# Performance work log

Hardware: AMD Instinct MI355X
Metric: run time of the kernel (lower is better)

The kernel has to match this reference:

```python
import jax, jax.numpy as jnp
import numpy as np

N_DIM = 512
HEADS = 8
NUM_EXPERTS = 65536
NUM_KEYS = 256      # sqrt(NUM_EXPERTS)
DIM_KEY = 256       # N_DIM // 2
TOPK = 16           # num_experts_per_head (also product_key_topk)
SCALE = 0.02


def setup_inputs() -> dict:
    key = jax.random.key(0)
    k0, k1, k2, k3, k4 = jax.random.split(key, 5)
    x = jax.random.normal(k0, (1, 2048, N_DIM), dtype=jnp.float32)
    W_q = jax.random.normal(k1, (N_DIM, 2 * HEADS * DIM_KEY), dtype=jnp.float32) * SCALE
    keys = jax.random.normal(k2, (HEADS, NUM_KEYS, 2, DIM_KEY), dtype=jnp.float32) * SCALE
    down_embed = jax.random.normal(k3, (NUM_EXPERTS, N_DIM), dtype=jnp.float32) * SCALE
    up_embed = jax.random.normal(k4, (NUM_EXPERTS, N_DIM), dtype=jnp.float32) * SCALE
    return {"x": x, "W_q": W_q, "keys": keys, "down_embed": down_embed, "up_embed": up_embed}


def reference(x, W_q, keys, down_embed, up_embed):
    b, n, d = x.shape
    # queries: [b,n,2*h*dk] -> [2,b,n,h,dk]
    q = (x @ W_q).reshape(b, n, 2, HEADS, DIM_KEY).transpose(2, 0, 1, 3, 4)
    # similarity against product keys: [2,b,n,h,num_keys]
    sim = jnp.einsum('pbnhd,hkpd->pbnhk', q, keys)
    sx, ix = jax.lax.top_k(sim[0], TOPK)   # [b,n,h,TOPK]
    sy, iy = jax.lax.top_k(sim[1], TOPK)
    # cartesian product of the two top-k sets -> [b,n,h,TOPK*TOPK]
    all_scores = (sx[..., :, None] + sy[..., None, :]).reshape(b, n, HEADS, TOPK * TOPK)
    scores, pk_idx = jax.lax.top_k(all_scores, TOPK)  # [b,n,h,TOPK]
    # NOTE: original module indexes embeddings with pk_idx (flat top-k positions),
    # reproduced faithfully here.
    w_down = down_embed[pk_idx]  # [b,n,h,TOPK,d]
    w_up = up_embed[pk_idx]      # [b,n,h,TOPK,d]
    h = jnp.einsum('bnd,bnhkd->bnhk', x, w_down)
    h = jax.nn.gelu(h, approximate=False)
    h = jax.nn.softmax(scores, axis=-1) * h
    return jnp.einsum('bnhk,bnhkd->bnd', h, w_up)
```

## Files before the change

kernel.cpp:

```cpp
#include <hip/hip_runtime.h>
#include <math.h>

#define N_TOK 2048
#define NDIM 512
#define HEADS 8
#define TOPK 16
#define QCOLS 4096
#define LSC 4096.0f
#define ILSC (1.0f/4096.0f)

typedef __attribute__((ext_vector_type(8))) _Float16 f16x8;
typedef __attribute__((ext_vector_type(4))) float f32x4;

__device__ __forceinline__ unsigned short f32_to_f16(float f) {
    _Float16 h = (_Float16)f;
    return __builtin_bit_cast(unsigned short, h);
}
__device__ __forceinline__ float f16_to_f32(unsigned short u) {
    return (float)__builtin_bit_cast(_Float16, u);
}
__device__ __forceinline__ void gl_lds16(const void* g, void* l) {
    __builtin_amdgcn_global_load_lds(
        (const __attribute__((address_space(1))) void*)g,
        (__attribute__((address_space(3))) void*)l, 16, 0, 0);
}

__device__ __forceinline__ void split_f4(const float* __restrict__ src,
                                         unsigned short* __restrict__ dh,
                                         unsigned short* __restrict__ dl,
                                         int i) {
    float4 v = reinterpret_cast<const float4*>(src)[i];
    float vv[4] = {v.x, v.y, v.z, v.w};
    ushort4 h, lo;
    unsigned short* hp = &h.x; unsigned short* lp = &lo.x;
    #pragma unroll
    for (int q = 0; q < 4; ++q) {
        unsigned short hh = f32_to_f16(vv[q]);
        hp[q] = hh;
        lp[q] = f32_to_f16((vv[q] - f16_to_f32(hh)) * LSC);
    }
    reinterpret_cast<ushort4*>(dh)[i] = h;
    reinterpret_cast<ushort4*>(dl)[i] = lo;
}

__global__ __launch_bounds__(256) void kP_split(const float* __restrict__ x,
                                                const float* __restrict__ Wq,
                                                const float* __restrict__ keys,
                                                const float* __restrict__ down,
                                                const float* __restrict__ up,
                                                unsigned short* __restrict__ xh,
                                                unsigned short* __restrict__ xl,
                                                unsigned short* __restrict__ Wqh,
                                                unsigned short* __restrict__ Wql,
                                                unsigned short* __restrict__ ksh,
                                                unsigned short* __restrict__ ksl,
                                                unsigned short* __restrict__ Mth,
                                                unsigned short* __restrict__ Mtl,
                                                unsigned short* __restrict__ upTh,
                                                unsigned short* __restrict__ upTl) {
    const int bid = blockIdx.x;
    const int tid = threadIdx.x;
    if (bid < 256) {
        #pragma unroll
        for (int t = 0; t < 4; ++t) split_f4(x, xh, xl, bid * 1024 + t * 256 + tid);
        return;
    }
    if (bid < 768) {
        const int b = bid - 256;
        #pragma unroll
        for (int t = 0; t < 4; ++t) split_f4(Wq, Wqh, Wql, b * 1024 + t * 256 + tid);
        return;
    }
    if (bid < 1024) {
        const int b = bid - 768;
        #pragma unroll
        for (int t = 0; t < 4; ++t) split_f4(keys, ksh, ksl, b * 1024 + t * 256 + tid);
        return;
    }
    if (bid < 1280) {
        const int e = bid - 1024;
        const int d0 = tid * 2;
        float2 v = *reinterpret_cast<const float2*>(&down[(size_t)e * NDIM + d0]);
        ushort2 h, lo;
        unsigned short h0 = f32_to_f16(v.x);
        unsigned short h1 = f32_to_f16(v.y);
        h.x = h0; h.y = h1;
        lo.x = f32_to_f16((v.x - f16_to_f32(h0)) * LSC);
        lo.y = f32_to_f16((v.y - f16_to_f32(h1)) * LSC);
        *reinterpret_cast<ushort2*>(&Mth[(size_t)(QCOLS + e) * NDIM + d0]) = h;
        *reinterpret_cast<ushort2*>(&Mtl[(size_t)(QCOLS + e) * NDIM + d0]) = lo;
        return;
    }
    const int b = bid - 1280;
    #pragma unroll
    for (int dd = 0; dd < 8; ++dd) {
        const int d = b * 8 + dd;
        const int e = tid;
        const float v = up[(size_t)e * NDIM + d];
        unsigned short hh = f32_to_f16(v);
        upTh[(size_t)d * 256 + e] = hh;
        upTl[(size_t)d * 256 + e] = f32_to_f16((v - f16_to_f32(hh)) * LSC);
    }
}

__global__ __launch_bounds__(256) void kQ_m1(const unsigned short* __restrict__ Wqh,
                                             const unsigned short* __restrict__ Wql,
                                             const unsigned short* __restrict__ ksh,
                                             const unsigned short* __restrict__ ksl,
                                             unsigned short* __restrict__ Mth,
                                             unsigned short* __restrict__ Mtl) {
    __shared__ __align__(16) char lds[36864];
    const int tid = threadIdx.x;
    const int w = tid >> 6, l = tid & 63;
    const int c0 = blockIdx.x * 32;
    const int ph = blockIdx.y;
    const int p = ph >> 3, h = ph & 7;
    const int off = p * 2048 + h * 256;
    f32x4 acch[2][4] = {};
    f32x4 accl[2][4] = {};

    for (int s = 0; s < 8; ++s) {
        const int kk = s * 32;
        __syncthreads();
        {
            const int q = w * 1024 + l * 16;
            const int r = q >> 7;
            const int bsw = (q & 127) ^ ((r & 7) << 4);
            const unsigned short* src = (bsw < 64)
                ? Wqh + (size_t)(c0 + r) * QCOLS + off + kk + (bsw >> 1)
                : Wql + (size_t)(c0 + r) * QCOLS + off + kk + ((bsw - 64) >> 1);
            gl_lds16(src, lds + w * 1024);
        }
        #pragma unroll
        for (int t = 0; t < 8; ++t) {
            const int q = w * 8192 + t * 1024 + l * 16;
            const int r = q >> 7;
            const int bsw = (q & 127) ^ ((r & 7) << 4);
            const unsigned short* src = (bsw < 64)
                ? ksh + ((size_t)(h * 256 + r) * 2 + p) * 256 + kk + (bsw >> 1)
                : ksl + ((size_t)(h * 256 + r) * 2 + p) * 256 + kk + ((bsw - 64) >> 1);
            gl_lds16(src, lds + 4096 + w * 8192 + t * 1024);
        }
        __syncthreads();
        const int bq = (l >> 4) * 16;
        f16x8 ah[2], al[2];
        #pragma unroll
        for (int mi = 0; mi < 2; ++mi) {
            const int ra = mi * 16 + (l & 15);
            const int swz = (ra & 7) << 4;
            ah[mi] = *(const f16x8*)(lds + ra * 128 + (bq ^ swz));
            al[mi] = *(const f16x8*)(lds + ra * 128 + ((bq + 64) ^ swz));
        }
        __builtin_amdgcn_s_setprio(1);
        #pragma unroll
        for (int nj = 0; nj < 4; ++nj) {
            const int rb = w * 64 + nj * 16 + (l & 15);
            const int swz = (rb & 7) << 4;
            f16x8 bh = *(const f16x8*)(lds + 4096 + rb * 128 + (bq ^ swz));
            f16x8 bl = *(const f16x8*)(lds + 4096 + rb * 128 + ((bq + 64) ^ swz));
            #pragma unroll
            for (int mi = 0; mi < 2; ++mi) {
                acch[mi][nj] = __builtin_amdgcn_mfma_f32_16x16x32_f16(ah[mi], bh, acch[mi][nj], 0, 0, 0);
                accl[mi][nj] = __builtin_amdgcn_mfma_f32_16x16x32_f16(ah[mi], bl, accl[mi][nj], 0, 0, 0);
                accl[mi][nj] = __builtin_amdgcn_mfma_f32_16x16x32_f16(al[mi], bh, accl[mi][nj], 0, 0, 0);
            }
        }
        __builtin_amdgcn_s_setprio(0);
    }
    #pragma unroll
    for (int mi = 0; mi < 2; ++mi)
        #pragma unroll
        for (int nj = 0; nj < 4; ++nj) {
            const int k = w * 64 + nj * 16 + (l & 15);
            const int cb = c0 + mi * 16 + (l >> 4) * 4;
            ushort4 h4, l4;
            unsigned short* hp = &h4.x; unsigned short* lp = &l4.x;
            #pragma unroll
            for (int r = 0; r < 4; ++r) {
                const float v = fmaf(accl[mi][nj][r], ILSC, acch[mi][nj][r]);
                unsigned short hh = f32_to_f16(v);
                hp[r] = hh;
                lp[r] = f32_to_f16((v - f16_to_f32(hh)) * LSC);
            }
            *reinterpret_cast<ushort4*>(&Mth[(size_t)(off + k) * NDIM + cb]) = h4;
            *reinterpret_cast<ushort4*>(&Mtl[(size_t)(off + k) * NDIM + cb]) = l4;
        }
}

#define BM 128
#define BN 128
#define BK 32
#define KFBUF 32768
__global__ __launch_bounds__(256, 2) void kF_gemm(const unsigned short* __restrict__ xh,
                                                  const unsigned short* __restrict__ xl,
                                                  const unsigned short* __restrict__ Mth,
                                                  const unsigned short* __restrict__ Mtl,
                                                  float* __restrict__ T,
                                                  float* __restrict__ D) {
    __shared__ __align__(16) char lds[2 * KFBUF];
    const int tid = threadIdx.x;
    const int w = tid >> 6, l = tid & 63;
    const int wm = w >> 1, wn = w & 1;
    const int orig = blockIdx.x;
    const int swz = (orig & 7) * 68 + (orig >> 3);
    const int by = swz >> 4;
    const int row0 = (swz & 15) * BM;
    const int colbase = by * 128;
    f32x4 acch[4][4] = {};
    f32x4 accl[4][4] = {};

    auto stage = [&](int buf, int s) {
        const int kk = s * BK;
        char* base = lds + buf * KFBUF;
        #pragma unroll
        for (int t = 0; t < 4; ++t) {
            const int q = w * 4096 + t * 1024 + l * 16;
            const int r = q >> 7;
            const int bsw = (q & 127) ^ ((r & 7) << 4);
            const unsigned short* src = (bsw < 64)
                ? xh + (size_t)(row0 + r) * NDIM + kk + (bsw >> 1)
                : xl + (size_t)(row0 + r) * NDIM + kk + ((bsw - 64) >> 1);
            gl_lds16(src, base + w * 4096 + t * 1024);
        }
        #pragma unroll
        for (int t = 0; t < 4; ++t) {
            const int q = w * 4096 + t * 1024 + l * 16;
            const int r = q >> 7;
            const int bsw = (q & 127) ^ ((r & 7) << 4);
            const unsigned short* src = (bsw < 64)
                ? Mth + (size_t)(colbase + r) * NDIM + kk + (bsw >> 1)
                : Mtl + (size_t)(colbase + r) * NDIM + kk + ((bsw - 64) >> 1);
            gl_lds16(src, base + 16384 + w * 4096 + t * 1024);
        }
    };

    stage(0, 0);
    __syncthreads();
    for (int s = 0; s < 16; ++s) {
        if (s + 1 < 16) stage((s + 1) & 1, s + 1);
        const char* base = lds + (s & 1) * KFBUF;
        const int bq = (l >> 4) * 16;
        f16x8 bh[4], bl[4];
        #pragma unroll
        for (int nj = 0; nj < 4; ++nj) {
            const int rb = wn * 64 + nj * 16 + (l & 15);
            const int sz = (rb & 7) << 4;
            bh[nj] = *(const f16x8*)(base + 16384 + rb * 128 + (bq ^ sz));
            bl[nj] = *(const f16x8*)(base + 16384 + rb * 128 + ((bq + 64) ^ sz));
        }
        __builtin_amdgcn_s_setprio(1);
        #pragma unroll
        for (int mi = 0; mi < 4; ++mi) {
            const int ra = wm * 64 + mi * 16 + (l & 15);
            const int sz = (ra & 7) << 4;
            f16x8 ah = *(const f16x8*)(base + ra * 128 + (bq ^ sz));
            f16x8 al = *(const f16x8*)(base + ra * 128 + ((bq + 64) ^ sz));
            #pragma unroll
            for (int nj = 0; nj < 4; ++nj) {
                acch[mi][nj] = __builtin_amdgcn_mfma_f32_16x16x32_f16(ah, bh[nj], acch[mi][nj], 0, 0, 0);
                accl[mi][nj] = __builtin_amdgcn_mfma_f32_16x16x32_f16(ah, bl[nj], accl[mi][nj], 0, 0, 0);
                accl[mi][nj] = __builtin_amdgcn_mfma_f32_16x16x32_f16(al, bh[nj], accl[mi][nj], 0, 0, 0);
            }
        }
        __builtin_amdgcn_s_setprio(0);
        __syncthreads();
    }

    if (by >= 32) {
        #pragma unroll
        for (int mi = 0; mi < 4; ++mi)
            #pragma unroll
            for (int nj = 0; nj < 4; ++nj)
                #pragma unroll
                for (int r = 0; r < 4; ++r) {
                    const int row = row0 + wm * 64 + mi * 16 + (l >> 4) * 4 + r;
                    const int col = (by - 32) * 128 + wn * 64 + nj * 16 + (l & 15);
                    D[(size_t)row * 256 + col] = fmaf(accl[mi][nj][r], ILSC, acch[mi][nj][r]);
                }
        return;
    }

    float* Cl = (float*)lds;
    const int grp8 = tid >> 3;
    const int lam8 = tid & 7;
    for (int c = 0; c < 4; ++c) {
        if (wm == (c >> 1)) {
            #pragma unroll
            for (int u = 0; u < 2; ++u) {
                const int mi = (c & 1) * 2 + u;
                #pragma unroll
                for (int nj = 0; nj < 4; ++nj)
                    #pragma unroll
                    for (int r = 0; r < 4; ++r)
                        Cl[(u * 16 + (l >> 4) * 4 + r) * 136 + wn * 64 + nj * 16 + (l & 15)] =
                            fmaf(accl[mi][nj][r], ILSC, acch[mi][nj][r]);
            }
        }
        __syncthreads();
        float v[16];
        #pragma unroll
        for (int j = 0; j < 16; ++j) v[j] = Cl[grp8 * 136 + lam8 + 8 * j];
        #pragma unroll
        for (int k = 2; k <= 16; k <<= 1)
            #pragma unroll
            for (int j = k >> 1; j > 0; j >>= 1)
                #pragma unroll
                for (int i = 0; i < 16; ++i) {
                    const int l2 = i ^ j;
                    if (l2 > i) {
                        const bool asc = ((i & k) == 0);
                        const float lo = fminf(v[i], v[l2]), hi = fmaxf(v[i], v[l2]);
                        v[i] = asc ? lo : hi;
                        v[l2] = asc ? hi : lo;
                    }
                }
        #pragma unroll
        for (int lvl = 1; lvl <= 4; lvl <<= 1) {
            float m[16];
            #pragma unroll
            for (int q = 0; q < 16; ++q)
                m[q] = fmaxf(v[q], __shfl_xor(v[15 - q], lvl));
            #pragma unroll
            for (int j = 8; j > 0; j >>= 1)
                #pragma unroll
                for (int i = 0; i < 16; ++i) {
                    const int l2 = i ^ j;
                    if (l2 > i) {
                        const float lo = fminf(m[i], m[l2]), hi = fmaxf(m[i], m[l2]);
                        m[i] = lo; m[l2] = hi;
                    }
                }
            #pragma unroll
            for (int q = 0; q < 16; ++q) v[q] = m[q];
        }
        const int n = row0 + c * 32 + grp8;
        T[((size_t)n * 32 + by) * 16 + 2 * lam8]     = v[15 - 2 * lam8];
        T[((size_t)n * 32 + by) * 16 + 2 * lam8 + 1] = v[14 - 2 * lam8];
        __syncthreads();
    }
}

__device__ const unsigned short CAND_TBL[32] = {
    0x0100, 0x0302, 0x0504, 0x0706, 0x0908, 0x0B0A, 0x0D0C, 0x0F0E,
    0x1110, 0x1312, 0x1514, 0x1716,
    0x2120, 0x2322, 0x3024, 0x3231, 0x4033, 0x4241,
    0x5150, 0x6160, 0x7170,
    0x9080, 0xB0A0, 0xD0C0, 0xF0E0,
    0xFFFF, 0xFFFF, 0xFFFF, 0xFFFF, 0xFFFF, 0xFFFF, 0xFFFF
};

__device__ __forceinline__ float sel16(const float a[16], int i) {
    float b0 = (i & 1) ? a[1] : a[0];
    float b1 = (i & 1) ? a[3] : a[2];
    float b2 = (i & 1) ? a[5] : a[4];
    float b3 = (i & 1) ? a[7] : a[6];
    float b4 = (i & 1) ? a[9] : a[8];
    float b5 = (i & 1) ? a[11] : a[10];
    float b6 = (i & 1) ? a[13] : a[12];
    float b7 = (i & 1) ? a[15] : a[14];
    float c0 = (i & 2) ? b1 : b0;
    float c1 = (i & 2) ? b3 : b2;
    float c2 = (i & 2) ? b5 : b4;
    float c3 = (i & 2) ? b7 : b6;
    float d0 = (i & 4) ? c1 : c0;
    float d1 = (i & 4) ? c3 : c2;
    return (i & 8) ? d1 : d0;
}

__device__ __forceinline__ void merge_desc16(const float* __restrict__ a,
                                             const float* __restrict__ b,
                                             float out_desc[16]) {
    float m[16];
    #pragma unroll
    for (int q = 0; q < 16; ++q) m[q] = fmaxf(a[q], b[15 - q]);
    #pragma unroll
    for (int k = 2; k <= 16; k <<= 1)
        #pragma unroll
        for (int j = k >> 1; j > 0; j >>= 1)
            #pragma unroll
            for (int i = 0; i < 16; ++i) {
                const int l2 = i ^ j;
                if (l2 > i) {
                    const bool asc = ((i & k) == 0);
                    const float lo = fminf(m[i], m[l2]), hi = fmaxf(m[i], m[l2]);
                    m[i] = asc ? lo : hi;
                    m[l2] = asc ? hi : lo;
                }
            }
    #pragma unroll
    for (int q = 0; q < 16; ++q) out_desc[q] = m[15 - q];
}

__global__ __launch_bounds__(256) void kC_combine(const float* __restrict__ T,
                                                  const float* __restrict__ D,
                                                  unsigned short* __restrict__ Wh,
                                                  unsigned short* __restrict__ Wl) {
    __shared__ unsigned long long ckey[8][50];
    __shared__ float winval[8][16];
    __shared__ int winflat[8][16];
    __shared__ int Wrow[256];

    const int tid = threadIdx.x;
    const int n = blockIdx.x;
    const int h = tid >> 5;
    const int lam = tid & 15;

    Wrow[tid] = 0;

    float a0[16], a1[16], b0v[16], b1v[16];
    const float* t00 = &T[((size_t)n * 32 + 2 * h) * 16];
    const float* t01 = &T[((size_t)n * 32 + 2 * h + 1) * 16];
    const float* t10 = &T[((size_t)n * 32 + 16 + 2 * h) * 16];
    const float* t11 = &T[((size_t)n * 32 + 17 + 2 * h) * 16];
    #pragma unroll
    for (int q = 0; q < 16; ++q) {
        a0[q] = t00[q]; a1[q] = t01[q];
        b0v[q] = t10[q]; b1v[q] = t11[q];
    }
    float sxd[16], syd[16];
    merge_desc16(a0, a1, sxd);
    merge_desc16(b0v, b1v, syd);

    const int lc = tid & 31;
    const unsigned int cw = CAND_TBL[lc];
    unsigned long long mykey[2]; float myval[2]; int myflat[2]; int myrank[2] = {0, 0};
    #pragma unroll
    for (int u = 0; u < 2; ++u) {
        const int fl = (cw >> (8 * u)) & 0xFF;
        const float sv = sel16(sxd, fl >> 4) + sel16(syd, fl & 15);
        const unsigned int uv = __float_as_uint(sv);
        const unsigned int mo = (uv & 0x80000000u) ? ~uv : (uv | 0x80000000u);
        mykey[u] = ((unsigned long long)mo << 8) | (unsigned long long)(255 - fl);
        myval[u] = sv; myflat[u] = fl;
        const int slot = lc * 2 + u;
        if (slot < 50) ckey[h][slot] = mykey[u];
    }
    __syncthreads();
    for (int kk = 0; kk < 50; ++kk) {
        const unsigned long long ok = ckey[h][kk];
        myrank[0] += (ok > mykey[0]) ? 1 : 0;
        myrank[1] += (ok > mykey[1]) ? 1 : 0;
    }
    #pragma unroll
    for (int u = 0; u < 2; ++u)
        if (myrank[u] < 16) { winval[h][myrank[u]] = myval[u]; winflat[h][myrank[u]] = myflat[u]; }
    __syncthreads();

    if (!(tid & 16)) {
        const float sc = winval[h][lam];
        const float m0 = winval[h][0];
        float e = expf(sc - m0);
        float esum = e;
        #pragma unroll
        for (int off = 1; off < 16; off <<= 1) esum += __shfl_xor(esum, off);
        const int fl = winflat[h][lam];
        const float hv = D[(size_t)n * 256 + fl];
        const float gg = 0.5f * hv * (1.0f + erff(hv * 0.70710678118654752f));
        const float wv = (e / esum) * gg;
        atomicAdd(&Wrow[fl], __float2int_rn(wv * 4194304.0f));
    }
    __syncthreads();
    const float wfin = (float)Wrow[tid] * (1.0f / 4194304.0f);
    const unsigned short hh = f32_to_f16(wfin);
    Wh[(size_t)n * 256 + tid] = hh;
    Wl[(size_t)n * 256 + tid] = f32_to_f16((wfin - f16_to_f32(hh)) * LSC);
}

__global__ __launch_bounds__(256) void k5_mfma(const unsigned short* __restrict__ Wh,
                                               const unsigned short* __restrict__ Wl,
                                               const unsigned short* __restrict__ upTh,
                                               const unsigned short* __restrict__ upTl,
                                               float* __restrict__ out) {
    __shared__ __align__(16) char lds[20480];
    const int tid = threadIdx.x;
    const int w = tid >> 6, l = tid & 63;
    const int n0 = blockIdx.x * 32;
    const int d0 = blockIdx.y * 128;
    f32x4 acch[2][2] = {};
    f32x4 accl[2][2] = {};

    for (int s = 0; s < 8; ++s) {
        const int kk = s * 32;
        __syncthreads();
        {
            const int q = w * 1024 + l * 16;
            const int r = q >> 7;
            const int bsw = (q & 127) ^ ((r & 7) << 4);
            const unsigned short* src = (bsw < 64)
                ? Wh + (size_t)(n0 + r) * 256 + kk + (bsw >> 1)
                : Wl + (size_t)(n0 + r) * 256 + kk + ((bsw - 64) >> 1);
            gl_lds16(src, lds + w * 1024);
        }
        #pragma unroll
        for (int t = 0; t < 4; ++t) {
            const int q = w * 4096 + t * 1024 + l * 16;
            const int r = q >> 7;
            const int bsw = (q & 127) ^ ((r & 7) << 4);
            const unsigned short* src = (bsw < 64)
                ? upTh + (size_t)(d0 + r) * 256 + kk + (bsw >> 1)
                : upTl + (size_t)(d0 + r) * 256 + kk + ((bsw - 64) >> 1);
            gl_lds16(src, lds + 4096 + w * 4096 + t * 1024);
        }
        __syncthreads();
        const int bq = (l >> 4) * 16;
        f16x8 ah[2], al[2];
        #pragma unroll
        for (int mi = 0; mi < 2; ++mi) {
            const int ra = mi * 16 + (l & 15);
            const int swz = (ra & 7) << 4;
            ah[mi] = *(const f16x8*)(lds + ra * 128 + (bq ^ swz));
            al[mi] = *(const f16x8*)(lds + ra * 128 + ((bq + 64) ^ swz));
        }
        #pragma unroll
        for (int nj = 0; nj < 2; ++nj) {
            const int rb = w * 32 + nj * 16 + (l & 15);
            const int swz = (rb & 7) << 4;
            f16x8 bh = *(const f16x8*)(lds + 4096 + rb * 128 + (bq ^ swz));
            f16x8 bl = *(const f16x8*)(lds + 4096 + rb * 128 + ((bq + 64) ^ swz));
            #pragma unroll
            for (int mi = 0; mi < 2; ++mi) {
                acch[mi][nj] = __builtin_amdgcn_mfma_f32_16x16x32_f16(ah[mi], bh, acch[mi][nj], 0, 0, 0);
                accl[mi][nj] = __builtin_amdgcn_mfma_f32_16x16x32_f16(ah[mi], bl, accl[mi][nj], 0, 0, 0);
                accl[mi][nj] = __builtin_amdgcn_mfma_f32_16x16x32_f16(al[mi], bh, accl[mi][nj], 0, 0, 0);
            }
        }
    }
    #pragma unroll
    for (int mi = 0; mi < 2; ++mi)
        #pragma unroll
        for (int nj = 0; nj < 2; ++nj)
            #pragma unroll
            for (int r = 0; r < 4; ++r) {
                const int row = n0 + mi * 16 + (l >> 4) * 4 + r;
                const int col = d0 + w * 32 + nj * 16 + (l & 15);
                out[(size_t)row * NDIM + col] = fmaf(accl[mi][nj][r], ILSC, acch[mi][nj][r]);
            }
}

extern "C" void kernel_launch(void* const* d_in, const int* in_sizes, int n_in,
                              void* d_out, int out_size, void* d_ws, size_t ws_size,
                              hipStream_t stream) {
    const float* x    = (const float*)d_in[0];
    const float* Wq   = (const float*)d_in[1];
    const float* keys = (const float*)d_in[2];
    const float* down = (const float*)d_in[3];
    const float* up   = (const float*)d_in[4];
    float* out = (float*)d_out;

    char* ws = (char*)d_ws;
    unsigned short* Mth  = (unsigned short*)(ws);
    unsigned short* Mtl  = (unsigned short*)(ws + 4456448);
    unsigned short* xh   = (unsigned short*)(ws + 8912896);
    unsigned short* xl   = (unsigned short*)(ws + 11010048);
    unsigned short* Wqh  = (unsigned short*)(ws + 13107200);
    unsigned short* Wql  = (unsigned short*)(ws + 17301504);
    unsigned short* ksh  = (unsigned short*)(ws + 21495808);
    unsigned short* ksl  = (unsigned short*)(ws + 23592960);
    unsigned short* upTh = (unsigned short*)(ws + 25690112);
    unsigned short* upTl = (unsigned short*)(ws + 25952256);
    float* T             = (float*)(ws + 26214400);
    float* D             = (float*)(ws + 30408704);
    unsigned short* Wh   = (unsigned short*)(ws + 32505856);
    unsigned short* Wl   = (unsigned short*)(ws + 33554432);

    kP_split<<<1344, 256, 0, stream>>>(x, Wq, keys, down, up,
                                       xh, xl, Wqh, Wql, ksh, ksl, Mth, Mtl, upTh, upTl);
    kQ_m1<<<dim3(16, 16), 256, 0, stream>>>(Wqh, Wql, ksh, ksl, Mth, Mtl);
    kF_gemm<<<544, 256, 0, stream>>>(xh, xl, Mth, Mtl, T, D);
    kC_combine<<<2048, 256, 0, stream>>>(T, D, Wh, Wl);
    k5_mfma<<<dim3(64, 4), 256, 0, stream>>>(Wh, Wl, upTh, upTl, out);
}
```

Baseline: 100.3 us.

## Pre-swizzle split-f16 operands into LDS tile layout and merge accumulators

Result: faster. 94.49 us (-5.8%).

```diff
diff --git a/kernel.cpp b/kernel.cpp
--- a/kernel.cpp
+++ b/kernel.cpp
@@ -25,10 +25,10 @@
         (__attribute__((address_space(3))) void*)l, 16, 0, 0);
 }
 
-__device__ __forceinline__ void split_f4(const float* __restrict__ src,
-                                         unsigned short* __restrict__ dh,
-                                         unsigned short* __restrict__ dl,
-                                         int i) {
+__device__ __forceinline__ void split_f4s(const float* __restrict__ src,
+                                          unsigned short* __restrict__ dh,
+                                          unsigned short* __restrict__ dl,
+                                          int i, float lsc) {
     float4 v = reinterpret_cast<const float4*>(src)[i];
     float vv[4] = {v.x, v.y, v.z, v.w};
     ushort4 h, lo;
@@ -37,7 +37,7 @@
     for (int q = 0; q < 4; ++q) {
         unsigned short hh = f32_to_f16(vv[q]);
         hp[q] = hh;
-        lp[q] = f32_to_f16((vv[q] - f16_to_f32(hh)) * LSC);
+        lp[q] = f32_to_f16((vv[q] - f16_to_f32(hh)) * lsc);
     }
     reinterpret_cast<ushort4*>(dh)[i] = h;
     reinterpret_cast<ushort4*>(dl)[i] = lo;
@@ -48,33 +48,51 @@
                                                 const float* __restrict__ keys,
                                                 const float* __restrict__ down,
                                                 const float* __restrict__ up,
-                                                unsigned short* __restrict__ xh,
-                                                unsigned short* __restrict__ xl,
+                                                char* __restrict__ xc,
                                                 unsigned short* __restrict__ Wqh,
                                                 unsigned short* __restrict__ Wql,
                                                 unsigned short* __restrict__ ksh,
                                                 unsigned short* __restrict__ ksl,
-                                                unsigned short* __restrict__ Mth,
-                                                unsigned short* __restrict__ Mtl,
+                                                char* __restrict__ Mc,
                                                 unsigned short* __restrict__ upTh,
                                                 unsigned short* __restrict__ upTl) {
     const int bid = blockIdx.x;
     const int tid = threadIdx.x;
     if (bid < 256) {
         #pragma unroll
-        for (int t = 0; t < 4; ++t) split_f4(x, xh, xl, bid * 1024 + t * 256 + tid);
+        for (int t = 0; t < 4; ++t) {
+            const int i = bid * 1024 + t * 256 + tid;
+            float4 v = reinterpret_cast<const float4*>(x)[i];
+            float vv[4] = {v.x, v.y, v.z, v.w};
+            ushort4 h, lo;
+            unsigned short* hp = &h.x; unsigned short* lp = &lo.x;
+            #pragma unroll
+            for (int q = 0; q < 4; ++q) {
+                unsigned short hh = f32_to_f16(vv[q]);
+                hp[q] = hh;
+                lp[q] = f32_to_f16(vv[q] - f16_to_f32(hh));
+            }
+            const int n = i >> 7;
+            const int k0 = (i & 127) * 4;
+            const int s = k0 >> 5;
+            const int o = (k0 & 31) * 2;
+            const int swz = (n & 7) << 4;
+            char* base = xc + ((size_t)s * 2048 + n) * 128;
+            *reinterpret_cast<ushort4*>(base + (o ^ swz)) = h;
+            *reinterpret_cast<ushort4*>(base + ((64 + o) ^ swz)) = lo;
+        }
         return;
     }
     if (bid < 768) {
         const int b = bid - 256;
         #pragma unroll
-        for (int t = 0; t < 4; ++t) split_f4(Wq, Wqh, Wql, b * 1024 + t * 256 + tid);
+        for (int t = 0; t < 4; ++t) split_f4s(Wq, Wqh, Wql, b * 1024 + t * 256 + tid, LSC);
         return;
     }
     if (bid < 1024) {
         const int b = bid - 768;
         #pragma unroll
-        for (int t = 0; t < 4; ++t) split_f4(keys, ksh, ksl, b * 1024 + t * 256 + tid);
+        for (int t = 0; t < 4; ++t) split_f4s(keys, ksh, ksl, b * 1024 + t * 256 + tid, LSC);
         return;
     }
     if (bid < 1280) {
@@ -85,10 +103,15 @@
         unsigned short h0 = f32_to_f16(v.x);
         unsigned short h1 = f32_to_f16(v.y);
         h.x = h0; h.y = h1;
-        lo.x = f32_to_f16((v.x - f16_to_f32(h0)) * LSC);
-        lo.y = f32_to_f16((v.y - f16_to_f32(h1)) * LSC);
-        *reinterpret_cast<ushort2*>(&Mth[(size_t)(QCOLS + e) * NDIM + d0]) = h;
-        *reinterpret_cast<ushort2*>(&Mtl[(size_t)(QCOLS + e) * NDIM + d0]) = lo;
+        lo.x = f32_to_f16(v.x - f16_to_f32(h0));
+        lo.y = f32_to_f16(v.y - f16_to_f32(h1));
+        const int s = d0 >> 5;
+        const int o = (d0 & 31) * 2;
+        const int mrow = QCOLS + e;
+        const int swz = (mrow & 7) << 4;
+        char* base = Mc + ((size_t)s * 4352 + mrow) * 128;
+        *reinterpret_cast<ushort2*>(base + (o ^ swz)) = h;
+        *reinterpret_cast<ushort2*>(base + ((64 + o) ^ swz)) = lo;
         return;
     }
     const int b = bid - 1280;
@@ -107,8 +130,7 @@
                                              const unsigned short* __restrict__ Wql,
                                              const unsigned short* __restrict__ ksh,
                                              const unsigned short* __restrict__ ksl,
-                                             unsigned short* __restrict__ Mth,
-                                             unsigned short* __restrict__ Mtl) {
+                                             char* __restrict__ Mc) {
     __shared__ __align__(16) char lds[36864];
     const int tid = threadIdx.x;
     const int w = tid >> 6, l = tid & 63;
@@ -180,10 +202,15 @@
                 const float v = fmaf(accl[mi][nj][r], ILSC, acch[mi][nj][r]);
                 unsigned short hh = f32_to_f16(v);
                 hp[r] = hh;
-                lp[r] = f32_to_f16((v - f16_to_f32(hh)) * LSC);
-            }
-            *reinterpret_cast<ushort4*>(&Mth[(size_t)(off + k) * NDIM + cb]) = h4;
-            *reinterpret_cast<ushort4*>(&Mtl[(size_t)(off + k) * NDIM + cb]) = l4;
+                lp[r] = f32_to_f16(v - f16_to_f32(hh));
+            }
+            const int mrow = off + k;
+            const int s2 = cb >> 5;
+            const int o = (cb & 31) * 2;
+            const int swz2 = (mrow & 7) << 4;
+            char* base = Mc + ((size_t)s2 * 4352 + mrow) * 128;
+            *reinterpret_cast<ushort4*>(base + (o ^ swz2)) = h4;
+            *reinterpret_cast<ushort4*>(base + ((64 + o) ^ swz2)) = l4;
         }
 }
 
@@ -191,10 +218,8 @@
 #define BN 128
 #define BK 32
 #define KFBUF 32768
-__global__ __launch_bounds__(256, 2) void kF_gemm(const unsigned short* __restrict__ xh,
-                                                  const unsigned short* __restrict__ xl,
-                                                  const unsigned short* __restrict__ Mth,
-                                                  const unsigned short* __restrict__ Mtl,
+__global__ __launch_bounds__(256, 2) void kF_gemm(const char* __restrict__ xc,
+                                                  const char* __restrict__ Mc,
                                                   float* __restrict__ T,
                                                   float* __restrict__ D) {
     __shared__ __align__(16) char lds[2 * KFBUF];
@@ -206,31 +231,16 @@
     const int by = swz >> 4;
     const int row0 = (swz & 15) * BM;
     const int colbase = by * 128;
-    f32x4 acch[4][4] = {};
-    f32x4 accl[4][4] = {};
+    f32x4 acc[4][4] = {};
 
     auto stage = [&](int buf, int s) {
-        const int kk = s * BK;
         char* base = lds + buf * KFBUF;
+        const char* asrc = xc + ((size_t)s * 2048 + row0) * 128;
+        const char* bsrc = Mc + ((size_t)s * 4352 + colbase) * 128;
         #pragma unroll
         for (int t = 0; t < 4; ++t) {
-            const int q = w * 4096 + t * 1024 + l * 16;
-            const int r = q >> 7;
-            const int bsw = (q & 127) ^ ((r & 7) << 4);
-            const unsigned short* src = (bsw < 64)
-                ? xh + (size_t)(row0 + r) * NDIM + kk + (bsw >> 1)
-                : xl + (size_t)(row0 + r) * NDIM + kk + ((bsw - 64) >> 1);
-            gl_lds16(src, base + w * 4096 + t * 1024);
-        }
-        #pragma unroll
-        for (int t = 0; t < 4; ++t) {
-            const int q = w * 4096 + t * 1024 + l * 16;
-            const int r = q >> 7;
-            const int bsw = (q & 127) ^ ((r & 7) << 4);
-            const unsigned short* src = (bsw < 64)
-                ? Mth + (size_t)(colbase + r) * NDIM + kk + (bsw >> 1)
-                : Mtl + (size_t)(colbase + r) * NDIM + kk + ((bsw - 64) >> 1);
-            gl_lds16(src, base + 16384 + w * 4096 + t * 1024);
+            gl_lds16(asrc + t * 4096 + tid * 16, base + t * 4096 + tid * 16);
+            gl_lds16(bsrc + t * 4096 + tid * 16, base + 16384 + t * 4096 + tid * 16);
         }
     };
 
@@ -257,9 +267,9 @@
             f16x8 al = *(const f16x8*)(base + ra * 128 + ((bq + 64) ^ sz));
             #pragma unroll
             for (int nj = 0; nj < 4; ++nj) {
-                acch[mi][nj] = __builtin_amdgcn_mfma_f32_16x16x32_f16(ah, bh[nj], acch[mi][nj], 0, 0, 0);
-                accl[mi][nj] = __builtin_amdgcn_mfma_f32_16x16x32_f16(ah, bl[nj], accl[mi][nj], 0, 0, 0);
-                accl[mi][nj] = __builtin_amdgcn_mfma_f32_16x16x32_f16(al, bh[nj], accl[mi][nj], 0, 0, 0);
+                acc[mi][nj] = __builtin_amdgcn_mfma_f32_16x16x32_f16(ah, bh[nj], acc[mi][nj], 0, 0, 0);
+                acc[mi][nj] = __builtin_amdgcn_mfma_f32_16x16x32_f16(ah, bl[nj], acc[mi][nj], 0, 0, 0);
+                acc[mi][nj] = __builtin_amdgcn_mfma_f32_16x16x32_f16(al, bh[nj], acc[mi][nj], 0, 0, 0);
             }
         }
         __builtin_amdgcn_s_setprio(0);
@@ -275,7 +285,7 @@
                 for (int r = 0; r < 4; ++r) {
                     const int row = row0 + wm * 64 + mi * 16 + (l >> 4) * 4 + r;
                     const int col = (by - 32) * 128 + wn * 64 + nj * 16 + (l & 15);
-                    D[(size_t)row * 256 + col] = fmaf(accl[mi][nj][r], ILSC, acch[mi][nj][r]);
+                    D[(size_t)row * 256 + col] = acc[mi][nj][r];
                 }
         return;
     }
@@ -283,6 +293,7 @@
     float* Cl = (float*)lds;
     const int grp8 = tid >> 3;
     const int lam8 = tid & 7;
+    #pragma unroll
     for (int c = 0; c < 4; ++c) {
         if (wm == (c >> 1)) {
             #pragma unroll
@@ -293,49 +304,51 @@
                     #pragma unroll
                     for (int r = 0; r < 4; ++r)
                         Cl[(u * 16 + (l >> 4) * 4 + r) * 136 + wn * 64 + nj * 16 + (l & 15)] =
-                            fmaf(accl[mi][nj][r], ILSC, acch[mi][nj][r]);
-            }
-        }
-        __syncthreads();
-        float v[16];
-        #pragma unroll
-        for (int j = 0; j < 16; ++j) v[j] = Cl[grp8 * 136 + lam8 + 8 * j];
-        #pragma unroll
-        for (int k = 2; k <= 16; k <<= 1)
-            #pragma unroll
-            for (int j = k >> 1; j > 0; j >>= 1)
+                            acc[mi][nj][r];
+            }
+        }
+        __syncthreads();
+        {
+            float v[16];
+            #pragma unroll
+            for (int j = 0; j < 16; ++j) v[j] = Cl[grp8 * 136 + lam8 + 8 * j];
+            #pragma unroll
+            for (int k = 2; k <= 16; k <<= 1)
                 #pragma unroll
-                for (int i = 0; i < 16; ++i) {
-                    const int l2 = i ^ j;
-                    if (l2 > i) {
-                        const bool asc = ((i & k) == 0);
-                        const float lo = fminf(v[i], v[l2]), hi = fmaxf(v[i], v[l2]);
-                        v[i] = asc ? lo : hi;
-                        v[l2] = asc ? hi : lo;
+                for (int j = k >> 1; j > 0; j >>= 1)
+                    #pragma unroll
+                    for (int i = 0; i < 16; ++i) {
+                        const int l2 = i ^ j;
+                        if (l2 > i) {
+                            const bool asc = ((i & k) == 0);
+                            const float lo = fminf(v[i], v[l2]), hi = fmaxf(v[i], v[l2]);
+                            v[i] = asc ? lo : hi;
+                            v[l2] = asc ? hi : lo;
+                        }
                     }
-                }
-        #pragma unroll
-        for (int lvl = 1; lvl <= 4; lvl <<= 1) {
-            float m[16];
-            #pragma unroll
-            for (int q = 0; q < 16; ++q)
-                m[q] = fmaxf(v[q], __shfl_xor(v[15 - q], lvl));
-            #pragma unroll
-            for (int j = 8; j > 0; j >>= 1)
+            #pragma unroll
+            for (int lvl = 1; lvl <= 4; lvl <<= 1) {
+                float m[16];
                 #pragma unroll
-                for (int i = 0; i < 16; ++i) {
-                    const int l2 = i ^ j;
-                    if (l2 > i) {
-                        const float lo = fminf(m[i], m[l2]), hi = fmaxf(m[i], m[l2]);
-                        m[i] = lo; m[l2] = hi;
+                for (int q = 0; q < 16; ++q)
+                    m[q] = fmaxf(v[q], __shfl_xor(v[15 - q], lvl));
+                #pragma unroll
+                for (int j = 8; j > 0; j >>= 1)
+                    #pragma unroll
+                    for (int i = 0; i < 16; ++i) {
+                        const int l2 = i ^ j;
+                        if (l2 > i) {
+                            const float lo = fminf(m[i], m[l2]), hi = fmaxf(m[i], m[l2]);
+                            m[i] = lo; m[l2] = hi;
+                        }
                     }
-                }
-            #pragma unroll
-            for (int q = 0; q < 16; ++q) v[q] = m[q];
-        }
-        const int n = row0 + c * 32 + grp8;
-        T[((size_t)n * 32 + by) * 16 + 2 * lam8]     = v[15 - 2 * lam8];
-        T[((size_t)n * 32 + by) * 16 + 2 * lam8 + 1] = v[14 - 2 * lam8];
+                #pragma unroll
+                for (int q = 0; q < 16; ++q) v[q] = m[q];
+            }
+            const int n = row0 + c * 32 + grp8;
+            T[((size_t)n * 32 + by) * 16 + 2 * lam8]     = v[15 - 2 * lam8];
+            T[((size_t)n * 32 + by) * 16 + 2 * lam8 + 1] = v[14 - 2 * lam8];
+        }
         __syncthreads();
     }
 }
@@ -548,10 +561,8 @@
     float* out = (float*)d_out;
 
     char* ws = (char*)d_ws;
-    unsigned short* Mth  = (unsigned short*)(ws);
-    unsigned short* Mtl  = (unsigned short*)(ws + 4456448);
-    unsigned short* xh   = (unsigned short*)(ws + 8912896);
-    unsigned short* xl   = (unsigned short*)(ws + 11010048);
+    char* Mc             = ws;
+    char* xc             = ws + 8912896;
     unsigned short* Wqh  = (unsigned short*)(ws + 13107200);
     unsigned short* Wql  = (unsigned short*)(ws + 17301504);
     unsigned short* ksh  = (unsigned short*)(ws + 21495808);
@@ -564,9 +575,9 @@
     unsigned short* Wl   = (unsigned short*)(ws + 33554432);
 
     kP_split<<<1344, 256, 0, stream>>>(x, Wq, keys, down, up,
-                                       xh, xl, Wqh, Wql, ksh, ksl, Mth, Mtl, upTh, upTl);
-    kQ_m1<<<dim3(16, 16), 256, 0, stream>>>(Wqh, Wql, ksh, ksl, Mth, Mtl);
-    kF_gemm<<<544, 256, 0, stream>>>(xh, xl, Mth, Mtl, T, D);
+                                       xc, Wqh, Wql, ksh, ksl, Mc, upTh, upTl);
+    kQ_m1<<<dim3(16, 16), 256, 0, stream>>>(Wqh, Wql, ksh, ksl, Mc);
+    kF_gemm<<<544, 256, 0, stream>>>(xc, Mc, T, D);
     kC_combine<<<2048, 256, 0, stream>>>(T, D, Wh, Wl);
     k5_mfma<<<dim3(64, 4), 256, 0, stream>>>(Wh, Wl, upTh, upTl, out);
 }
```
